# Kernel tuning notes

Hardware: AMD Instinct MI355X
Metric: run time of the kernel (lower is better)

The kernel has to match this reference:

```python
import jax, jax.numpy as jnp
import numpy as np

B, N_FED, INPUT_DIM, LATENT_DIM = 8192, 16384, 1024, 512


def setup_inputs() -> dict:
    key = jax.random.key(0)
    k1, k2, k3 = jax.random.split(key, 3)
    enc = jax.random.normal(k1, (B, LATENT_DIM), dtype=jnp.float32)
    X_fed = jax.random.normal(k2, (N_FED, INPUT_DIM), dtype=jnp.float32)
    # torch.rand -> uniform [0, 1)
    domain_diff = jax.random.uniform(k3, (INPUT_DIM, LATENT_DIM), dtype=jnp.float32)
    return {"enc": enc, "X_fed": X_fed, "domain_diff": domain_diff}


def reference(enc, X_fed, domain_diff):
    # K = V = X_fed @ domain_diff  (computed once; torch source computes it twice)
    kv = X_fed @ domain_diff                      # (N_fed, latent)
    scores = jnp.einsum('bd,nd->bn', enc, kv) / enc.shape[1]  # scale by latent_dim
    attn = jax.nn.softmax(scores, axis=1)         # softmax over N_fed axis
    z = attn @ kv                                 # (B, latent)
    return z
```

## Files before the change

kernel.cpp:

```cpp
#include <hip/hip_runtime.h>
#include <hip/hip_bf16.h>
#include <stdint.h>

#define ENC_B 8192
#define NFED  16384
#define INDIM 1024
#define LAT   512
#define SCALE (1.0f/512.0f)

typedef __attribute__((ext_vector_type(4))) float f32x4;
typedef __attribute__((ext_vector_type(8))) short short8;
typedef __attribute__((ext_vector_type(4))) short short4_t;

static __device__ __forceinline__ short f2bf(float x){
  union { float f; uint32_t u; } v; v.f = x;
  uint32_t r = v.u + 0x7FFFu + ((v.u >> 16) & 1u);
  return (short)(r >> 16);
}
static __device__ __forceinline__ float bf2f(short s){
  union { float f; uint32_t u; } v; v.u = ((uint32_t)(unsigned short)s) << 16; return v.f;
}

static __device__ __forceinline__ void gload16(const void* g, void* l){
  __builtin_amdgcn_global_load_lds(
      (const __attribute__((address_space(1))) void*)g,
      (__attribute__((address_space(3))) void*)l, 16, 0, 0);
}

__global__ void ddT_kernel(const float* __restrict__ dd, short* __restrict__ ddT){
  const int n = blockIdx.x;
  for (int k = threadIdx.x; k < INDIM; k += 256)
    ddT[(size_t)n*INDIM + k] = f2bf(dd[(size_t)k*LAT + n]);
}

__global__ __launch_bounds__(256) void encb_kernel(const float* __restrict__ enc,
                                                   short* __restrict__ encb){
  const int gid = blockIdx.x*256 + threadIdx.x;
  const size_t base = (size_t)gid * 8;
  float4 v0 = *(const float4*)(enc + base);
  float4 v1 = *(const float4*)(enc + base + 4);
  short8 s;
  s[0]=f2bf(v0.x*SCALE); s[1]=f2bf(v0.y*SCALE); s[2]=f2bf(v0.z*SCALE); s[3]=f2bf(v0.w*SCALE);
  s[4]=f2bf(v1.x*SCALE); s[5]=f2bf(v1.y*SCALE); s[6]=f2bf(v1.z*SCALE); s[7]=f2bf(v1.w*SCALE);
  *(short8*)(encb + base) = s;
}

__global__ __launch_bounds__(256, 4) void kv_gemm_kernel(const float* __restrict__ X,
                                                         const short* __restrict__ ddT,
                                                         short* __restrict__ kv){
  __shared__ __align__(16) char lds[32768 + 512];
  short* As = (short*)lds;
  float* Bs = (float*)(lds + 8192);
  const int t = threadIdx.x;
  const int lane = t & 63, w = t >> 6;
  const int lr = lane & 15, lg = lane >> 4;
  const int n0 = blockIdx.x * 128;
  const int m0 = blockIdx.y * 128;

  const short* asrc[2];
  #pragma unroll
  for (int i=0;i<2;++i){
    int ca = i*256 + w*64 + lane;
    int row = ca >> 2;
    int c  = (lane & 3) ^ (row & 3) ^ ((row >> 2) & 3);
    asrc[i] = ddT + (size_t)(n0 + row)*INDIM + c*8;
  }
  const float* bsrc[4];
  #pragma unroll
  for (int i=0;i<4;++i){
    int ca = i*256 + w*64 + lane;
    int row = ca >> 3;
    int c  = (lane & 7) ^ (row & 7);
    bsrc[i] = X + (size_t)(m0 + row)*INDIM + c*4;
  }

  f32x4 acc[2][8];
  #pragma unroll
  for (int i=0;i<2;++i)
    #pragma unroll
    for (int j=0;j<8;++j) acc[i][j] = (f32x4){0.f,0.f,0.f,0.f};

  for (int ks = 0; ks < 32; ++ks){
    #pragma unroll
    for (int i=0;i<2;++i){
      gload16(asrc[i], (char*)As + i*4096 + w*1024);
      asrc[i] += 32;
    }
    #pragma unroll
    for (int i=0;i<4;++i){
      gload16(bsrc[i], (char*)Bs + i*4096 + w*1024);
      bsrc[i] += 32;
    }
    __syncthreads();

    short8 b[2];
    #pragma unroll
    for (int ri=0;ri<2;++ri){
      int row = w*32 + ri*16 + lr;
      uint32_t sw = ((uint32_t)(row & 7)) << 4;
      f32x4 f0 = *(const f32x4*)((char*)Bs + row*128 + ((uint32_t)(lg*32) ^ sw));
      f32x4 f1 = *(const f32x4*)((char*)Bs + row*128 + ((uint32_t)(lg*32 + 16) ^ sw));
      short8 s;
      s[0]=f2bf(f0[0]); s[1]=f2bf(f0[1]); s[2]=f2bf(f0[2]); s[3]=f2bf(f0[3]);
      s[4]=f2bf(f1[0]); s[5]=f2bf(f1[1]); s[6]=f2bf(f1[2]); s[7]=f2bf(f1[3]);
      b[ri] = s;
    }
    #pragma unroll
    for (int h=0;h<2;++h){
      short8 a[4];
      #pragma unroll
      for (int j=0;j<4;++j){
        int row = (h*4 + j)*16 + lr;
        uint32_t c = (uint32_t)(lg ^ (row & 3) ^ ((row >> 2) & 3));
        a[j] = *(short8*)((char*)As + row*64 + c*16);
      }
      #pragma unroll
      for (int ri=0;ri<2;++ri)
        #pragma unroll
        for (int j=0;j<4;++j)
          acc[ri][h*4+j] = __builtin_amdgcn_mfma_f32_16x16x32_bf16(a[j], b[ri], acc[ri][h*4+j], 0,0,0);
    }
    __syncthreads();
  }

  char* Pt = lds;
  #pragma unroll
  for (int ri=0;ri<2;++ri){
    const int m = w*32 + ri*16 + lr;
    const uint32_t rswz = ((uint32_t)(m & 7)) << 4;
    #pragma unroll
    for (int dj=0;dj<8;++dj){
      short4_t pv;
      #pragma unroll
      for (int r=0;r<4;++r) pv[r] = f2bf(acc[ri][dj][r]);
      *(short4_t*)(Pt + m*256 + (((uint32_t)(dj*32 + lg*8)) ^ rswz)) = pv;
    }
  }
  __syncthreads();
  #pragma unroll
  for (int i=0;i<8;++i){
    uint32_t c = (uint32_t)(i*256 + t);
    uint32_t row = c >> 4, c16 = c & 15;
    short8 v = *(short8*)(Pt + row*256 + ((c16*16) ^ (((uint32_t)(row & 7)) << 4)));
    *(short8*)(kv + (size_t)(m0 + row)*LAT + n0 + c16*8) = v;
  }
}

__global__ __launch_bounds__(256) void kvT_kernel(const short* __restrict__ kv,
                                                  short* __restrict__ kvT){
  __shared__ short tile[64][72];
  const int t = threadIdx.x;
  const int bn = blockIdx.x & (NFED/64 - 1);
  const int bd = blockIdx.x / (NFED/64);
  #pragma unroll
  for (int i=0;i<2;++i){
    int idx = t + i*256; int row = idx >> 3, cc = (idx & 7)*8;
    *(uint4*)&tile[row][cc] = *(const uint4*)(kv + (size_t)(bn*64+row)*LAT + bd*64 + cc);
  }
  __syncthreads();
  #pragma unroll
  for (int i=0;i<2;++i){
    int idx = t + i*256; int drow = idx >> 3, nn = (idx & 7)*8;
    short8 v;
    #pragma unroll
    for (int j=0;j<8;++j) v[j] = tile[nn+j][drow];
    *(short8*)(kvT + (size_t)(bd*64+drow)*NFED + bn*64 + nn) = v;
  }
}

__global__ __launch_bounds__(256, 4) void s_gemm_kernel(const short* __restrict__ encb,
                                                        const short* __restrict__ kv,
                                                        short* __restrict__ Pc,
                                                        float* __restrict__ lpart,
                                                        int cbase, int chunk){
  __shared__ __align__(16) char lds[32768 + 512];
  short* As = (short*)lds;
  short* Bs = (short*)(lds + 16384);
  const int t = threadIdx.x;
  const int lane = t & 63, w = t >> 6;
  const int lr = lane & 15, lg = lane >> 4;
  const int n0g = cbase + blockIdx.x * 128;
  const int m0  = blockIdx.y * 128;

  const short* asrc[4]; const short* bsrc[4];
  #pragma unroll
  for (int i=0;i<4;++i){
    int ca = i*256 + w*64 + lane;
    int row = ca >> 3;
    int kcs = (lane & 7) ^ (row & 7);
    asrc[i] = kv   + (size_t)(n0g + row)*LAT + kcs*8;
    bsrc[i] = encb + (size_t)(m0  + row)*LAT + kcs*8;
  }

  f32x4 acc[2][8];
  #pragma unroll
  for (int i=0;i<2;++i)
    #pragma unroll
    for (int j=0;j<8;++j) acc[i][j] = (f32x4){0.f,0.f,0.f,0.f};

  for (int ks = 0; ks < 8; ++ks){
    #pragma unroll
    for (int i=0;i<4;++i){
      gload16(asrc[i], (char*)As + i*4096 + w*1024);
      gload16(bsrc[i], (char*)Bs + i*4096 + w*1024);
      asrc[i] += 64; bsrc[i] += 64;
    }
    __syncthreads();

    #pragma unroll
    for (int kk=0;kk<2;++kk){
      const uint32_t kbyte = (uint32_t)(kk*64 + lg*16);
      short8 b[2];
      #pragma unroll
      for (int ri=0;ri<2;++ri){
        int row = w*32 + ri*16 + lr;
        b[ri] = *(short8*)((char*)Bs + row*128 + (kbyte ^ ((uint32_t)(row & 7) << 4)));
      }
      #pragma unroll
      for (int h=0;h<2;++h){
        short8 a[4];
        #pragma unroll
        for (int j=0;j<4;++j){
          int row = (h*4 + j)*16 + lr;
          a[j] = *(short8*)((char*)As + row*128 + (kbyte ^ ((uint32_t)(row & 7) << 4)));
        }
        #pragma unroll
        for (int ri=0;ri<2;++ri)
          #pragma unroll
          for (int j=0;j<4;++j)
            acc[ri][h*4+j] = __builtin_amdgcn_mfma_f32_16x16x32_bf16(a[j], b[ri], acc[ri][h*4+j], 0,0,0);
      }
    }
    __syncthreads();
  }

  char*  Pt   = lds;
  float* lsum = (float*)(lds + 32768);
  #pragma unroll
  for (int ri=0;ri<2;++ri){
    const int q = w*32 + ri*16 + lr;
    const uint32_t rswz = ((uint32_t)(q & 7)) << 4;
    float ps = 0.f;
    #pragma unroll
    for (int dj=0;dj<8;++dj){
      short4_t pv;
      #pragma unroll
      for (int r=0;r<4;++r){
        float pe = __expf(acc[ri][dj][r]);
        ps += pe;
        pv[r] = f2bf(pe);
      }
      *(short4_t*)(Pt + q*256 + (((uint32_t)(dj*32 + lg*8)) ^ rswz)) = pv;
    }
    ps += __shfl_xor(ps, 16, 64);
    ps += __shfl_xor(ps, 32, 64);
    if (lg == 0) lsum[q] = ps;
  }
  __syncthreads();
  #pragma unroll
  for (int i=0;i<8;++i){
    uint32_t c = (uint32_t)(i*256 + t);
    uint32_t row = c >> 4, c16 = c & 15;
    short8 v = *(short8*)(Pt + row*256 + ((c16*16) ^ (((uint32_t)(row & 7)) << 4)));
    *(short8*)(Pc + (size_t)(m0 + row)*chunk + blockIdx.x*128 + c16*8) = v;
  }
  if (t < 128){
    int jsl = (cbase >> 7) + blockIdx.x;
    lpart[(size_t)jsl*ENC_B + m0 + t] = lsum[t];
  }
}

__global__ __launch_bounds__(256, 4) void z_gemm_kernel(const short* __restrict__ kvT,
                                                        const short* __restrict__ Pc,
                                                        short* __restrict__ zb,
                                                        int cbase, int chunk,
                                                        int sliceBase, int first){
  __shared__ __align__(16) short As[64*64];
  __shared__ __align__(16) short Bs[128*64];
  const int t = threadIdx.x;
  const int lane = t & 63, w = t >> 6;
  const int lr = lane & 15, lg = lane >> 4;
  const int n0 = blockIdx.x * 128;
  const int m0 = blockIdx.y * 64;
  const int s  = blockIdx.z;
  const int sl = sliceBase + s;
  const int klocal0 = s * (chunk >> 1);

  const short* Asrc[2];
  #pragma unroll
  for (int i=0;i<2;++i){
    int ca = i*256 + w*64 + lane;
    int row = ca >> 3;
    int kcs = (lane & 7) ^ (row & 7);
    Asrc[i] = kvT + (size_t)(m0 + row)*NFED + cbase + klocal0 + kcs*8;
  }
  const short* Bsrc[4];
  #pragma unroll
  for (int i=0;i<4;++i){
    int ca = i*256 + w*64 + lane;
    int row = ca >> 3;
    int kcs = (lane & 7) ^ (row & 7);
    Bsrc[i] = Pc + (size_t)(n0 + row)*chunk + klocal0 + kcs*8;
  }

  f32x4 acc[2][4];
  #pragma unroll
  for (int i=0;i<2;++i)
    #pragma unroll
    for (int j=0;j<4;++j) acc[i][j] = (f32x4){0.f,0.f,0.f,0.f};

  const int ksteps = chunk >> 7;
  for (int ks = 0; ks < ksteps; ++ks) {
    #pragma unroll
    for (int i=0;i<2;++i){
      gload16(Asrc[i], (char*)As + i*4096 + w*1024);
      Asrc[i] += 64;
    }
    #pragma unroll
    for (int i=0;i<4;++i){
      gload16(Bsrc[i], (char*)Bs + i*4096 + w*1024);
      Bsrc[i] += 64;
    }
    __syncthreads();

    #pragma unroll
    for (int kk=0;kk<2;++kk){
      const uint32_t kbyte = kk*64 + lg*16;
      short8 a[4], b[2];
      #pragma unroll
      for (int dj=0;dj<4;++dj){
        int row = dj*16 + lr;
        a[dj] = *(short8*)((char*)As + row*128 + (kbyte ^ ((uint32_t)(row & 7) << 4)));
      }
      #pragma unroll
      for (int ri=0;ri<2;++ri){
        int row = w*32 + ri*16 + lr;
        b[ri] = *(short8*)((char*)Bs + row*128 + (kbyte ^ ((uint32_t)(row & 7) << 4)));
      }
      #pragma unroll
      for (int ri=0;ri<2;++ri)
        #pragma unroll
        for (int dj=0;dj<4;++dj)
          acc[ri][dj] = __builtin_amdgcn_mfma_f32_16x16x32_bf16(a[dj], b[ri], acc[ri][dj], 0,0,0);
    }
    __syncthreads();
  }

  #pragma unroll
  for (int ri=0;ri<2;++ri)
    #pragma unroll
    for (int dj=0;dj<4;++dj)
      #pragma unroll
      for (int r=0;r<4;++r) {
        int d    = m0 + dj*16 + lg*4 + r;
        int rowq = n0 + w*32 + ri*16 + lr;
        size_t idx = ((size_t)sl*LAT + d)*ENC_B + rowq;
        float v = acc[ri][dj][r];
        if (!first) v += bf2f(zb[idx]);
        zb[idx] = f2bf(v);
      }
}

__global__ __launch_bounds__(256) void lred_kernel(const float* __restrict__ lpart,
                                                   float* __restrict__ linv){
  const int row = blockIdx.x*256 + threadIdx.x;
  float sum = 0.f;
  for (int j = 0; j < NFED/128; ++j)
    sum += lpart[(size_t)j*ENC_B + row];
  linv[row] = 1.0f / sum;
}

__global__ __launch_bounds__(256) void zcomb_kernel(const short* __restrict__ zb,
                                                    const float* __restrict__ linv,
                                                    float* __restrict__ out){
  __shared__ float tile[64][65];
  const int t = threadIdx.x;
  const int bx = blockIdx.x;
  const int by = blockIdx.y;
  #pragma unroll
  for (int i=0;i<4;++i){
    int idx = t + i*256;
    int dr = idx >> 4, rc = (idx & 15)*4;
    float s0=0.f, s1=0.f, s2=0.f, s3=0.f;
    #pragma unroll
    for (int sl=0; sl<8; ++sl){
      short4_t v = *(const short4_t*)(zb + ((size_t)sl*LAT + by*64 + dr)*ENC_B + bx*64 + rc);
      s0 += bf2f(v[0]); s1 += bf2f(v[1]); s2 += bf2f(v[2]); s3 += bf2f(v[3]);
    }
    tile[dr][rc+0]=s0; tile[dr][rc+1]=s1; tile[dr][rc+2]=s2; tile[dr][rc+3]=s3;
  }
  __syncthreads();
  #pragma unroll
  for (int i=0;i<4;++i){
    int idx = t + i*256;
    int rr = idx >> 4, dc = (idx & 15)*4;
    float li = linv[bx*64 + rr];
    float4 o;
    o.x = tile[dc+0][rr]*li; o.y = tile[dc+1][rr]*li;
    o.z = tile[dc+2][rr]*li; o.w = tile[dc+3][rr]*li;
    *(float4*)(out + (size_t)(bx*64+rr)*LAT + by*64 + dc) = o;
  }
}

extern "C" void kernel_launch(void* const* d_in, const int* in_sizes, int n_in,
                              void* d_out, int out_size, void* d_ws, size_t ws_size,
                              hipStream_t stream) {
  const float* enc = (const float*)d_in[0];
  const float* X   = (const float*)d_in[1];
  const float* dd  = (const float*)d_in[2];
  float* out = (float*)d_out;

  short* kvb   = (short*)d_ws;
  short* kvT   = (short*)((char*)d_ws + 16777216);
  short* encb  = (short*)((char*)d_ws + 33554432);
  float* lpart = (float*)((char*)d_ws + 41943040);
  short* ddT   = (short*)((char*)d_ws + 41943040);
  float* linv  = (float*)((char*)d_ws + 46137344);
  short* zb    = (short*)((char*)d_ws + 50331648);
  short* Pc    = (short*)((char*)d_ws + 117440512);

  int chunk;
  if      (ws_size >= (size_t)117440512 + (size_t)4096*ENC_B*2) chunk = 4096;
  else if (ws_size >= (size_t)117440512 + (size_t)2048*ENC_B*2) chunk = 2048;
  else                                                          chunk = 1024;

  ddT_kernel<<<LAT, 256, 0, stream>>>(dd, ddT);
  kv_gemm_kernel<<<dim3(LAT/128, NFED/128), 256, 0, stream>>>(X, ddT, kvb);
  kvT_kernel<<<(NFED/64)*(LAT/64), 256, 0, stream>>>(kvb, kvT);
  encb_kernel<<<ENC_B*LAT/(256*8), 256, 0, stream>>>(enc, encb);

  const int nc = NFED / chunk;
  for (int c = 0; c < nc; ++c) {
    s_gemm_kernel<<<dim3(chunk/128, ENC_B/128), 256, 0, stream>>>(
        encb, kvb, Pc, lpart, c*chunk, chunk);
    z_gemm_kernel<<<dim3(ENC_B/128, LAT/64, 2), 256, 0, stream>>>(
        kvT, Pc, zb, c*chunk, chunk, (c & 3)*2, (c < 4) ? 1 : 0);
  }
  lred_kernel<<<ENC_B/256, 256, 0, stream>>>(lpart, linv);
  zcomb_kernel<<<dim3(ENC_B/64, LAT/64), 256, 0, stream>>>(zb, linv, out);
}
```

Measured before the change: 417.9 us.

## Pre-convert X to bf16 and add XCD-aware block swizzle to GEMMs

```diff
diff --git a/kernel.cpp b/kernel.cpp
--- a/kernel.cpp
+++ b/kernel.cpp
@@ -25,6 +25,10 @@
   __builtin_amdgcn_global_load_lds(
       (const __attribute__((address_space(1))) void*)g,
       (__attribute__((address_space(3))) void*)l, 16, 0, 0);
+}
+
+static __device__ __forceinline__ int xcd_swz(int lid, int nwg){
+  return (lid & 7) * (nwg >> 3) + (lid >> 3);
 }
 
 __global__ void ddT_kernel(const float* __restrict__ dd, short* __restrict__ ddT){
@@ -45,142 +49,32 @@
   *(short8*)(encb + base) = s;
 }
 
-__global__ __launch_bounds__(256, 4) void kv_gemm_kernel(const float* __restrict__ X,
+__global__ __launch_bounds__(256) void xb_kernel(const float* __restrict__ X,
+                                                 short* __restrict__ Xb){
+  const int gid = blockIdx.x*256 + threadIdx.x;
+  const size_t base = (size_t)gid * 8;
+  float4 v0 = *(const float4*)(X + base);
+  float4 v1 = *(const float4*)(X + base + 4);
+  short8 s;
+  s[0]=f2bf(v0.x); s[1]=f2bf(v0.y); s[2]=f2bf(v0.z); s[3]=f2bf(v0.w);
+  s[4]=f2bf(v1.x); s[5]=f2bf(v1.y); s[6]=f2bf(v1.z); s[7]=f2bf(v1.w);
+  *(short8*)(Xb + base) = s;
+}
+
+__global__ __launch_bounds__(256, 4) void kv_gemm_kernel(const short* __restrict__ Xb,
                                                          const short* __restrict__ ddT,
                                                          short* __restrict__ kv){
-  __shared__ __align__(16) char lds[32768 + 512];
-  short* As = (short*)lds;
-  float* Bs = (float*)(lds + 8192);
-  const int t = threadIdx.x;
-  const int lane = t & 63, w = t >> 6;
-  const int lr = lane & 15, lg = lane >> 4;
-  const int n0 = blockIdx.x * 128;
-  const int m0 = blockIdx.y * 128;
-
-  const short* asrc[2];
-  #pragma unroll
-  for (int i=0;i<2;++i){
-    int ca = i*256 + w*64 + lane;
-    int row = ca >> 2;
-    int c  = (lane & 3) ^ (row & 3) ^ ((row >> 2) & 3);
-    asrc[i] = ddT + (size_t)(n0 + row)*INDIM + c*8;
-  }
-  const float* bsrc[4];
-  #pragma unroll
-  for (int i=0;i<4;++i){
-    int ca = i*256 + w*64 + lane;
-    int row = ca >> 3;
-    int c  = (lane & 7) ^ (row & 7);
-    bsrc[i] = X + (size_t)(m0 + row)*INDIM + c*4;
-  }
-
-  f32x4 acc[2][8];
-  #pragma unroll
-  for (int i=0;i<2;++i)
-    #pragma unroll
-    for (int j=0;j<8;++j) acc[i][j] = (f32x4){0.f,0.f,0.f,0.f};
-
-  for (int ks = 0; ks < 32; ++ks){
-    #pragma unroll
-    for (int i=0;i<2;++i){
-      gload16(asrc[i], (char*)As + i*4096 + w*1024);
-      asrc[i] += 32;
-    }
-    #pragma unroll
-    for (int i=0;i<4;++i){
-      gload16(bsrc[i], (char*)Bs + i*4096 + w*1024);
-      bsrc[i] += 32;
-    }
-    __syncthreads();
-
-    short8 b[2];
-    #pragma unroll
-    for (int ri=0;ri<2;++ri){
-      int row = w*32 + ri*16 + lr;
-      uint32_t sw = ((uint32_t)(row & 7)) << 4;
-      f32x4 f0 = *(const f32x4*)((char*)Bs + row*128 + ((uint32_t)(lg*32) ^ sw));
-      f32x4 f1 = *(const f32x4*)((char*)Bs + row*128 + ((uint32_t)(lg*32 + 16) ^ sw));
-      short8 s;
-      s[0]=f2bf(f0[0]); s[1]=f2bf(f0[1]); s[2]=f2bf(f0[2]); s[3]=f2bf(f0[3]);
-      s[4]=f2bf(f1[0]); s[5]=f2bf(f1[1]); s[6]=f2bf(f1[2]); s[7]=f2bf(f1[3]);
-      b[ri] = s;
-    }
-    #pragma unroll
-    for (int h=0;h<2;++h){
-      short8 a[4];
-      #pragma unroll
-      for (int j=0;j<4;++j){
-        int row = (h*4 + j)*16 + lr;
-        uint32_t c = (uint32_t)(lg ^ (row & 3) ^ ((row >> 2) & 3));
-        a[j] = *(short8*)((char*)As + row*64 + c*16);
-      }
-      #pragma unroll
-      for (int ri=0;ri<2;++ri)
-        #pragma unroll
-        for (int j=0;j<4;++j)
-          acc[ri][h*4+j] = __builtin_amdgcn_mfma_f32_16x16x32_bf16(a[j], b[ri], acc[ri][h*4+j], 0,0,0);
-    }
-    __syncthreads();
-  }
-
-  char* Pt = lds;
-  #pragma unroll
-  for (int ri=0;ri<2;++ri){
-    const int m = w*32 + ri*16 + lr;
-    const uint32_t rswz = ((uint32_t)(m & 7)) << 4;
-    #pragma unroll
-    for (int dj=0;dj<8;++dj){
-      short4_t pv;
-      #pragma unroll
-      for (int r=0;r<4;++r) pv[r] = f2bf(acc[ri][dj][r]);
-      *(short4_t*)(Pt + m*256 + (((uint32_t)(dj*32 + lg*8)) ^ rswz)) = pv;
-    }
-  }
-  __syncthreads();
-  #pragma unroll
-  for (int i=0;i<8;++i){
-    uint32_t c = (uint32_t)(i*256 + t);
-    uint32_t row = c >> 4, c16 = c & 15;
-    short8 v = *(short8*)(Pt + row*256 + ((c16*16) ^ (((uint32_t)(row & 7)) << 4)));
-    *(short8*)(kv + (size_t)(m0 + row)*LAT + n0 + c16*8) = v;
-  }
-}
-
-__global__ __launch_bounds__(256) void kvT_kernel(const short* __restrict__ kv,
-                                                  short* __restrict__ kvT){
-  __shared__ short tile[64][72];
-  const int t = threadIdx.x;
-  const int bn = blockIdx.x & (NFED/64 - 1);
-  const int bd = blockIdx.x / (NFED/64);
-  #pragma unroll
-  for (int i=0;i<2;++i){
-    int idx = t + i*256; int row = idx >> 3, cc = (idx & 7)*8;
-    *(uint4*)&tile[row][cc] = *(const uint4*)(kv + (size_t)(bn*64+row)*LAT + bd*64 + cc);
-  }
-  __syncthreads();
-  #pragma unroll
-  for (int i=0;i<2;++i){
-    int idx = t + i*256; int drow = idx >> 3, nn = (idx & 7)*8;
-    short8 v;
-    #pragma unroll
-    for (int j=0;j<8;++j) v[j] = tile[nn+j][drow];
-    *(short8*)(kvT + (size_t)(bd*64+drow)*NFED + bn*64 + nn) = v;
-  }
-}
-
-__global__ __launch_bounds__(256, 4) void s_gemm_kernel(const short* __restrict__ encb,
-                                                        const short* __restrict__ kv,
-                                                        short* __restrict__ Pc,
-                                                        float* __restrict__ lpart,
-                                                        int cbase, int chunk){
   __shared__ __align__(16) char lds[32768 + 512];
   short* As = (short*)lds;
   short* Bs = (short*)(lds + 16384);
   const int t = threadIdx.x;
   const int lane = t & 63, w = t >> 6;
   const int lr = lane & 15, lg = lane >> 4;
-  const int n0g = cbase + blockIdx.x * 128;
-  const int m0  = blockIdx.y * 128;
+  const int nwg = gridDim.x * gridDim.y;
+  const int nid = xcd_swz(blockIdx.x + gridDim.x*blockIdx.y, nwg);
+  const int bx = nid % gridDim.x, by = nid / gridDim.x;
+  const int n0 = bx * 128;
+  const int m0 = by * 128;
 
   const short* asrc[4]; const short* bsrc[4];
   #pragma unroll
@@ -188,8 +82,8 @@
     int ca = i*256 + w*64 + lane;
     int row = ca >> 3;
     int kcs = (lane & 7) ^ (row & 7);
-    asrc[i] = kv   + (size_t)(n0g + row)*LAT + kcs*8;
-    bsrc[i] = encb + (size_t)(m0  + row)*LAT + kcs*8;
+    asrc[i] = ddT + (size_t)(n0 + row)*INDIM + kcs*8;
+    bsrc[i] = Xb  + (size_t)(m0 + row)*INDIM + kcs*8;
   }
 
   f32x4 acc[2][8];
@@ -198,7 +92,7 @@
     #pragma unroll
     for (int j=0;j<8;++j) acc[i][j] = (f32x4){0.f,0.f,0.f,0.f};
 
-  for (int ks = 0; ks < 8; ++ks){
+  for (int ks = 0; ks < 16; ++ks){
     #pragma unroll
     for (int i=0;i<4;++i){
       gload16(asrc[i], (char*)As + i*4096 + w*1024);
@@ -234,6 +128,120 @@
     __syncthreads();
   }
 
+  char* Pt = lds;
+  #pragma unroll
+  for (int ri=0;ri<2;++ri){
+    const int m = w*32 + ri*16 + lr;
+    const uint32_t rswz = ((uint32_t)(m & 7)) << 4;
+    #pragma unroll
+    for (int dj=0;dj<8;++dj){
+      short4_t pv;
+      #pragma unroll
+      for (int r=0;r<4;++r) pv[r] = f2bf(acc[ri][dj][r]);
+      *(short4_t*)(Pt + m*256 + (((uint32_t)(dj*32 + lg*8)) ^ rswz)) = pv;
+    }
+  }
+  __syncthreads();
+  #pragma unroll
+  for (int i=0;i<8;++i){
+    uint32_t c = (uint32_t)(i*256 + t);
+    uint32_t row = c >> 4, c16 = c & 15;
+    short8 v = *(short8*)(Pt + row*256 + ((c16*16) ^ (((uint32_t)(row & 7)) << 4)));
+    *(short8*)(kv + (size_t)(m0 + row)*LAT + n0 + c16*8) = v;
+  }
+}
+
+__global__ __launch_bounds__(256) void kvT_kernel(const short* __restrict__ kv,
+                                                  short* __restrict__ kvT){
+  __shared__ short tile[64][72];
+  const int t = threadIdx.x;
+  const int bn = blockIdx.x & (NFED/64 - 1);
+  const int bd = blockIdx.x / (NFED/64);
+  #pragma unroll
+  for (int i=0;i<2;++i){
+    int idx = t + i*256; int row = idx >> 3, cc = (idx & 7)*8;
+    *(uint4*)&tile[row][cc] = *(const uint4*)(kv + (size_t)(bn*64+row)*LAT + bd*64 + cc);
+  }
+  __syncthreads();
+  #pragma unroll
+  for (int i=0;i<2;++i){
+    int idx = t + i*256; int drow = idx >> 3, nn = (idx & 7)*8;
+    short8 v;
+    #pragma unroll
+    for (int j=0;j<8;++j) v[j] = tile[nn+j][drow];
+    *(short8*)(kvT + (size_t)(bd*64+drow)*NFED + bn*64 + nn) = v;
+  }
+}
+
+__global__ __launch_bounds__(256, 4) void s_gemm_kernel(const short* __restrict__ encb,
+                                                        const short* __restrict__ kv,
+                                                        short* __restrict__ Pc,
+                                                        float* __restrict__ lpart,
+                                                        int cbase, int chunk){
+  __shared__ __align__(16) char lds[32768 + 512];
+  short* As = (short*)lds;
+  short* Bs = (short*)(lds + 16384);
+  const int t = threadIdx.x;
+  const int lane = t & 63, w = t >> 6;
+  const int lr = lane & 15, lg = lane >> 4;
+  const int nwg = gridDim.x * gridDim.y;
+  const int nid = xcd_swz(blockIdx.x + gridDim.x*blockIdx.y, nwg);
+  const int bx = nid % gridDim.x, by = nid / gridDim.x;
+  const int n0g = cbase + bx * 128;
+  const int m0  = by * 128;
+
+  const short* asrc[4]; const short* bsrc[4];
+  #pragma unroll
+  for (int i=0;i<4;++i){
+    int ca = i*256 + w*64 + lane;
+    int row = ca >> 3;
+    int kcs = (lane & 7) ^ (row & 7);
+    asrc[i] = kv   + (size_t)(n0g + row)*LAT + kcs*8;
+    bsrc[i] = encb + (size_t)(m0  + row)*LAT + kcs*8;
+  }
+
+  f32x4 acc[2][8];
+  #pragma unroll
+  for (int i=0;i<2;++i)
+    #pragma unroll
+    for (int j=0;j<8;++j) acc[i][j] = (f32x4){0.f,0.f,0.f,0.f};
+
+  for (int ks = 0; ks < 8; ++ks){
+    #pragma unroll
+    for (int i=0;i<4;++i){
+      gload16(asrc[i], (char*)As + i*4096 + w*1024);
+      gload16(bsrc[i], (char*)Bs + i*4096 + w*1024);
+      asrc[i] += 64; bsrc[i] += 64;
+    }
+    __syncthreads();
+
+    #pragma unroll
+    for (int kk=0;kk<2;++kk){
+      const uint32_t kbyte = (uint32_t)(kk*64 + lg*16);
+      short8 b[2];
+      #pragma unroll
+      for (int ri=0;ri<2;++ri){
+        int row = w*32 + ri*16 + lr;
+        b[ri] = *(short8*)((char*)Bs + row*128 + (kbyte ^ ((uint32_t)(row & 7) << 4)));
+      }
+      #pragma unroll
+      for (int h=0;h<2;++h){
+        short8 a[4];
+        #pragma unroll
+        for (int j=0;j<4;++j){
+          int row = (h*4 + j)*16 + lr;
+          a[j] = *(short8*)((char*)As + row*128 + (kbyte ^ ((uint32_t)(row & 7) << 4)));
+        }
+        #pragma unroll
+        for (int ri=0;ri<2;++ri)
+          #pragma unroll
+          for (int j=0;j<4;++j)
+            acc[ri][h*4+j] = __builtin_amdgcn_mfma_f32_16x16x32_bf16(a[j], b[ri], acc[ri][h*4+j], 0,0,0);
+      }
+    }
+    __syncthreads();
+  }
+
   char*  Pt   = lds;
   float* lsum = (float*)(lds + 32768);
   #pragma unroll
@@ -262,10 +270,10 @@
     uint32_t c = (uint32_t)(i*256 + t);
     uint32_t row = c >> 4, c16 = c & 15;
     short8 v = *(short8*)(Pt + row*256 + ((c16*16) ^ (((uint32_t)(row & 7)) << 4)));
-    *(short8*)(Pc + (size_t)(m0 + row)*chunk + blockIdx.x*128 + c16*8) = v;
+    *(short8*)(Pc + (size_t)(m0 + row)*chunk + bx*128 + c16*8) = v;
   }
   if (t < 128){
-    int jsl = (cbase >> 7) + blockIdx.x;
+    int jsl = (cbase >> 7) + bx;
     lpart[(size_t)jsl*ENC_B + m0 + t] = lsum[t];
   }
 }
@@ -280,9 +288,14 @@
   const int t = threadIdx.x;
   const int lane = t & 63, w = t >> 6;
   const int lr = lane & 15, lg = lane >> 4;
-  const int n0 = blockIdx.x * 128;
-  const int m0 = blockIdx.y * 64;
-  const int s  = blockIdx.z;
+  const int nwg = gridDim.x * gridDim.y * gridDim.z;
+  const int nid = xcd_swz(blockIdx.x + gridDim.x*(blockIdx.y + gridDim.y*blockIdx.z), nwg);
+  const int bx = nid % gridDim.x;
+  const int rem = nid / gridDim.x;
+  const int by = rem % gridDim.y;
+  const int s  = rem / gridDim.y;
+  const int n0 = bx * 128;
+  const int m0 = by * 64;
   const int sl = sliceBase + s;
   const int klocal0 = s * (chunk >> 1);
 
@@ -417,6 +430,7 @@
   short* ddT   = (short*)((char*)d_ws + 41943040);
   float* linv  = (float*)((char*)d_ws + 46137344);
   short* zb    = (short*)((char*)d_ws + 50331648);
+  short* Xb    = (short*)((char*)d_ws + 50331648);
   short* Pc    = (short*)((char*)d_ws + 117440512);
 
   int chunk;
@@ -425,7 +439,8 @@
   else                                                          chunk = 1024;
 
   ddT_kernel<<<LAT, 256, 0, stream>>>(dd, ddT);
-  kv_gemm_kernel<<<dim3(LAT/128, NFED/128), 256, 0, stream>>>(X, ddT, kvb);
+  xb_kernel<<<NFED*INDIM/(256*8), 256, 0, stream>>>(X, Xb);
+  kv_gemm_kernel<<<dim3(LAT/128, NFED/128), 256, 0, stream>>>(Xb, ddT, kvb);
   kvT_kernel<<<(NFED/64)*(LAT/64), 256, 0, stream>>>(kvb, kvT);
   encb_kernel<<<ENC_B*LAT/(256*8), 256, 0, stream>>>(enc, encb);
 
```

Measured after the change: 561.7 us. 34.4% more time.
